# Kernel tuning notes

Measured on AMD Instinct MI355X. Metric: run time of the kernel, lower is better.

## Reference

```python
import jax, jax.numpy as jnp
import numpy as np

SINKHORN_ITERS = 5
EPS_CLAMP = 1e-8   # matches torch eps=1e-08 in unbalanced_optimal_transport
EPS_COS = 1e-6     # matches cosine_distance eps
EPS_DIV = 1e-6     # matches weighted_ref / rigid transform eps


def setup_inputs() -> dict:
    key = jax.random.key(0)
    k0, k1, k2, k3 = jax.random.split(key, 4)
    B, D, M, N = 32, 512, 1024, 1024
    return {
        "src_embedding": jax.random.normal(k0, (B, D, M), dtype=jnp.float32),
        "tgt_embedding": jax.random.normal(k1, (B, D, N), dtype=jnp.float32),
        "src": jax.random.normal(k2, (B, 3, M), dtype=jnp.float32),
        "tgt": jax.random.normal(k3, (B, 3, N), dtype=jnp.float32),
        "l": jnp.float32(1.0),    # learned scalar nn.Parameter
        "rho": jnp.float32(1.0),  # learned scalar nn.Parameter
    }


def reference(src_embedding, tgt_embedding, src, tgt, l, rho):
    # ---- batched cosine distance: C[b] = 1 - <x1, x2> / (|x1||x2|) ----
    x1 = jnp.swapaxes(src_embedding, 1, 2)  # (B, M, D)
    x2 = jnp.swapaxes(tgt_embedding, 1, 2)  # (B, N, D)
    w1 = jnp.linalg.norm(x1, axis=2, keepdims=True)  # (B, M, 1)
    w2 = jnp.linalg.norm(x2, axis=2, keepdims=True)  # (B, N, 1)
    denom = jnp.clip(w1 * jnp.swapaxes(w2, 1, 2), EPS_COS, None)
    C = 1.0 - jnp.einsum('bmd,bnd->bmn', x1, x2) / denom  # (B, M, N)

    # ---- batched unbalanced Sinkhorn (5 fixed iterations) ----
    B, M, N = C.shape
    a = jnp.float32(1.0 / M)
    b = jnp.float32(1.0 / N)
    K = jnp.exp(-C / jnp.clip(l, EPS_CLAMP, None))        # (B, M, N)
    fi = rho / jnp.clip(rho + l, EPS_CLAMP, None)
    v = jnp.full((B, N), b, dtype=C.dtype)
    u = jnp.full((B, M), a, dtype=C.dtype)
    for _ in range(SINKHORN_ITERS):
        u = (a / jnp.clip(jnp.einsum('bmn,bn->bm', K, v), EPS_CLAMP, None)) ** fi
        v = (b / jnp.clip(jnp.einsum('bmn,bm->bn', K, u), EPS_CLAMP, None)) ** fi
    P = u[:, :, None] * K * v[:, None, :]                  # transport plan (B, M, N)

    # ---- soft correspondences ----
    row = jnp.sum(P, axis=2)                               # (B, M)
    tgt_pts = jnp.swapaxes(tgt, 1, 2)                      # (B, N, 3)
    weighted_ref = jnp.einsum('bmn,bnd->bmd', P, tgt_pts) / (row[:, :, None] + EPS_DIV)

    # ---- weighted Kabsch rigid transform (batched 3x3 SVD) ----
    a_pts = jnp.swapaxes(src, 1, 2)                        # (B, M, 3)
    w = row[:, :, None] / (jnp.sum(row, axis=1)[:, None, None] + EPS_DIV)  # (B, M, 1)
    centroid_a = jnp.sum(a_pts * w, axis=1)                # (B, 3)
    centroid_b = jnp.sum(weighted_ref * w, axis=1)         # (B, 3)
    a_c = a_pts - centroid_a[:, None, :]
    b_c = weighted_ref - centroid_b[:, None, :]
    cov = jnp.einsum('bmi,bmj->bij', a_c, b_c * w)         # (B, 3, 3)

    U, S, Vh = jnp.linalg.svd(cov, full_matrices=True)
    V = jnp.swapaxes(Vh, 1, 2)                             # torch.svd returns V, not V^T
    Ut = jnp.swapaxes(U, 1, 2)
    rot_pos = V @ Ut
    rot_neg = V.at[:, :, 2].multiply(-1.0) @ Ut            # flip last column of V
    det = jnp.linalg.det(rot_pos)[:, None, None]
    R = jnp.where(det > 0, rot_pos, rot_neg)               # (B, 3, 3)
    t = -jnp.einsum('bij,bj->bi', R, centroid_a) + centroid_b  # (B, 3)
    return R, t, P
```

## Files before the change

kernel.cpp:

```cpp
#include <hip/hip_runtime.h>
#include <math.h>

#define BB 32
#define DD 512
#define MM 1024
#define NN 1024

typedef float f32x4 __attribute__((ext_vector_type(4)));
typedef _Float16 f16x8 __attribute__((ext_vector_type(8)));

__global__ __launch_bounds__(256)
void norms_init_kernel(const float* __restrict__ srcE, const float* __restrict__ tgtE,
                       float* __restrict__ w1, float* __restrict__ w2,
                       float* __restrict__ v, float* __restrict__ colsum)
{
    const int idx = blockIdx.x * 256 + threadIdx.x;
    const float* e; float* w; int r;
    if (idx < 32768) {
        e = srcE; w = w1; r = idx;
        v[idx] = 1.0f / 1024.0f;
        colsum[idx] = 0.0f;
    } else {
        e = tgtE; w = w2; r = idx - 32768;
    }
    const int b = r >> 10;
    const int m = r & 1023;
    const float* p = e + (size_t)b * (DD * MM) + m;
    float acc = 0.f;
    #pragma unroll 8
    for (int d = 0; d < DD; ++d) {
        const float x = p[(size_t)d * MM];
        acc = fmaf(x, x, acc);
    }
    w[r] = sqrtf(acc);
}

__global__ __launch_bounds__(256)
void gemm_kexp_kernel(const float* __restrict__ Ae, const float* __restrict__ Be,
                      const float* __restrict__ w1, const float* __restrict__ w2,
                      const float* __restrict__ lp, float* __restrict__ Kout)
{
    __shared__ _Float16 As[128 * 64];
    __shared__ _Float16 Bs[128 * 64];

    const int tid  = threadIdx.x;
    const int lane = tid & 63;
    const int wave = tid >> 6;
    const int m0 = blockIdx.x * 128;
    const int n0 = blockIdx.y * 128;
    const int b  = blockIdx.z;
    const int wm = (wave & 1) * 64;
    const int wn = (wave >> 1) * 64;
    const int m16  = lane & 15;
    const int quad = lane >> 4;

    const float* Ab = Ae + (size_t)b * DD * MM;
    const float* Bb = Be + (size_t)b * DD * NN;

    f32x4 acc[4][4];
    #pragma unroll
    for (int i = 0; i < 4; ++i)
        #pragma unroll
        for (int j = 0; j < 4; ++j)
            acc[i][j] = (f32x4){0.f, 0.f, 0.f, 0.f};

    const int sm = tid & 127;
    const int kh = tid >> 7;
    const int sw = sm & 7;
    const float* apBase = Ab + m0 + sm;
    const float* bpBase = Bb + n0 + sm;

    float av[4][8], bv[4][8];
    #pragma unroll
    for (int t = 0; t < 4; ++t) {
        const int kg = kh + 2 * t;
        const float* ap = apBase + (size_t)(kg * 8) * MM;
        const float* bp = bpBase + (size_t)(kg * 8) * NN;
        #pragma unroll
        for (int j = 0; j < 8; ++j) { av[t][j] = ap[(size_t)j * MM]; bv[t][j] = bp[(size_t)j * NN]; }
    }

    for (int kt = 0; kt < 8; ++kt) {
        f16x8 pa[4], pb[4];
        #pragma unroll
        for (int t = 0; t < 4; ++t)
            #pragma unroll
            for (int j = 0; j < 8; ++j) { pa[t][j] = (_Float16)av[t][j]; pb[t][j] = (_Float16)bv[t][j]; }
        if (kt) __syncthreads();
        #pragma unroll
        for (int t = 0; t < 4; ++t) {
            const int kg = kh + 2 * t;
            const int off = sm * 64 + ((kg ^ sw) << 3);
            *reinterpret_cast<f16x8*>(&As[off]) = pa[t];
            *reinterpret_cast<f16x8*>(&Bs[off]) = pb[t];
        }
        __syncthreads();
        if (kt < 7) {
            const size_t kbase = (size_t)(kt + 1) * 64;
            #pragma unroll
            for (int t = 0; t < 4; ++t) {
                const int kg = kh + 2 * t;
                const float* ap = apBase + (kbase + kg * 8) * MM;
                const float* bp = bpBase + (kbase + kg * 8) * NN;
                #pragma unroll
                for (int j = 0; j < 8; ++j) { av[t][j] = ap[(size_t)j * MM]; bv[t][j] = bp[(size_t)j * NN]; }
            }
        }
        #pragma unroll
        for (int ks = 0; ks < 2; ++ks) {
            const int kg = ks * 4 + quad;
            f16x8 af[4], bfr[4];
            #pragma unroll
            for (int i = 0; i < 4; ++i) {
                const int rm = wm + i * 16 + m16;
                af[i]  = *reinterpret_cast<const f16x8*>(&As[rm * 64 + ((kg ^ (rm & 7)) << 3)]);
                const int rn = wn + i * 16 + m16;
                bfr[i] = *reinterpret_cast<const f16x8*>(&Bs[rn * 64 + ((kg ^ (rn & 7)) << 3)]);
            }
            #pragma unroll
            for (int i = 0; i < 4; ++i)
                #pragma unroll
                for (int j = 0; j < 4; ++j)
                    acc[i][j] = __builtin_amdgcn_mfma_f32_16x16x32_f16(af[i], bfr[j], acc[i][j], 0, 0, 0);
        }
    }

    const float inv_l = 1.0f / fmaxf(lp[0], 1e-8f);
    float w2v[4];
    #pragma unroll
    for (int j = 0; j < 4; ++j) w2v[j] = w2[b * NN + n0 + wn + j * 16 + m16];
    float* Kb = Kout + ((size_t)b << 20);
    #pragma unroll
    for (int i = 0; i < 4; ++i) {
        #pragma unroll
        for (int r = 0; r < 4; ++r) {
            const int m = m0 + wm + i * 16 + quad * 4 + r;
            const float w1v = w1[b * MM + m];
            #pragma unroll
            for (int j = 0; j < 4; ++j) {
                const float dot = acc[i][j][r];
                const float den = fmaxf(w1v * w2v[j], 1e-6f);
                const float kv  = __expf((dot / den - 1.0f) * inv_l);
                Kb[(size_t)m * NN + (n0 + wn + j * 16 + m16)] = kv;
            }
        }
    }
}

__global__ __launch_bounds__(256)
void uv_fused_kernel(const float* __restrict__ Kmat, const float* __restrict__ v,
                     float* __restrict__ u, float* __restrict__ colsum,
                     const float* __restrict__ lp, const float* __restrict__ rp)
{
    const int ms = blockIdx.x;
    const int b  = blockIdx.y;
    const int wv = threadIdx.x >> 6, lane = threadIdx.x & 63;
    const float l = lp[0], rho = rp[0];
    const float fi = rho / fmaxf(rho + l, 1e-8f);

    const float4* vb = reinterpret_cast<const float4*>(v + (b << 10));
    float4 vreg[4];
    #pragma unroll
    for (int c = 0; c < 4; ++c) vreg[c] = vb[c * 64 + lane];

    float4 cacc[4];
    #pragma unroll
    for (int c = 0; c < 4; ++c) cacc[c] = (float4){0.f, 0.f, 0.f, 0.f};

    const int m0 = ms * 32 + wv * 8;
    const float4* Kb = reinterpret_cast<const float4*>(Kmat + ((size_t)b << 20));
    float* ub = u + (b << 10);

    #pragma unroll
    for (int g = 0; g < 2; ++g) {
        float4 k4[4][4];
        #pragma unroll
        for (int r = 0; r < 4; ++r) {
            const int m = m0 + g * 4 + r;
            const float4* row = Kb + (size_t)m * 256;
            #pragma unroll
            for (int c = 0; c < 4; ++c) k4[r][c] = row[c * 64 + lane];
        }
        float s[4];
        #pragma unroll
        for (int r = 0; r < 4; ++r) {
            float t = 0.f;
            #pragma unroll
            for (int c = 0; c < 4; ++c) {
                t = fmaf(k4[r][c].x, vreg[c].x, t);
                t = fmaf(k4[r][c].y, vreg[c].y, t);
                t = fmaf(k4[r][c].z, vreg[c].z, t);
                t = fmaf(k4[r][c].w, vreg[c].w, t);
            }
            s[r] = t;
        }
        #pragma unroll
        for (int off = 32; off > 0; off >>= 1)
            #pragma unroll
            for (int r = 0; r < 4; ++r) s[r] += __shfl_down(s[r], off);
        float um[4];
        #pragma unroll
        for (int r = 0; r < 4; ++r) {
            const float sv = __builtin_amdgcn_readfirstlane(s[r]);
            um[r] = __powf((1.0f / 1024.0f) / fmaxf(sv, 1e-8f), fi);
        }
        if (lane == 0) {
            #pragma unroll
            for (int r = 0; r < 4; ++r) ub[m0 + g * 4 + r] = um[r];
        }
        #pragma unroll
        for (int r = 0; r < 4; ++r)
            #pragma unroll
            for (int c = 0; c < 4; ++c) {
                cacc[c].x = fmaf(k4[r][c].x, um[r], cacc[c].x);
                cacc[c].y = fmaf(k4[r][c].y, um[r], cacc[c].y);
                cacc[c].z = fmaf(k4[r][c].z, um[r], cacc[c].z);
                cacc[c].w = fmaf(k4[r][c].w, um[r], cacc[c].w);
            }
    }

    __shared__ float4 red[4][256];
    #pragma unroll
    for (int c = 0; c < 4; ++c) red[wv][c * 64 + lane] = cacc[c];
    __syncthreads();
    const int t = threadIdx.x;
    float4 s4 = red[0][t];
    #pragma unroll
    for (int w = 1; w < 4; ++w) {
        s4.x += red[w][t].x; s4.y += red[w][t].y;
        s4.z += red[w][t].z; s4.w += red[w][t].w;
    }
    float* cs = colsum + (b << 10) + t * 4;
    atomicAdd(cs + 0, s4.x);
    atomicAdd(cs + 1, s4.y);
    atomicAdd(cs + 2, s4.z);
    atomicAdd(cs + 3, s4.w);
}

__global__ __launch_bounds__(256)
void v_finalize_kernel(float* __restrict__ colsum, float* __restrict__ v,
                       const float* __restrict__ lp, const float* __restrict__ rp)
{
    const int idx = blockIdx.x * 256 + threadIdx.x;
    const float s = colsum[idx];
    colsum[idx] = 0.0f;
    const float l = lp[0], rho = rp[0];
    const float fi = rho / fmaxf(rho + l, 1e-8f);
    v[idx] = __powf((1.0f / 1024.0f) / fmaxf(s, 1e-8f), fi);
}

__global__ __launch_bounds__(256)
void p_pass_kernel(float* __restrict__ Kmat, const float* __restrict__ u,
                   const float* __restrict__ v, const float* __restrict__ tgt,
                   float* __restrict__ rowb, float* __restrict__ wref)
{
    const int gid  = (blockIdx.x * 256 + threadIdx.x) >> 6;
    const int lane = threadIdx.x & 63;
    const int b = gid >> 10;
    float4* row = reinterpret_cast<float4*>(Kmat + ((size_t)gid << 10));
    const float4* vb = reinterpret_cast<const float4*>(v + (b << 10));
    const float4* tb = reinterpret_cast<const float4*>(tgt + (size_t)b * 3072);
    const float um = u[gid];
    float4 s4 = {0,0,0,0}, x4 = {0,0,0,0}, y4 = {0,0,0,0}, z4 = {0,0,0,0};
    #pragma unroll
    for (int it = 0; it < 4; ++it) {
        const int i = it * 64 + lane;
        const float4 k4 = row[i];
        const float4 v4 = vb[i];
        float4 p;
        p.x = um * k4.x * v4.x;
        p.y = um * k4.y * v4.y;
        p.z = um * k4.z * v4.z;
        p.w = um * k4.w * v4.w;
        row[i] = p;
        const float4 tx = tb[i], ty = tb[256 + i], tz = tb[512 + i];
        s4.x += p.x; s4.y += p.y; s4.z += p.z; s4.w += p.w;
        x4.x = fmaf(p.x, tx.x, x4.x); x4.y = fmaf(p.y, tx.y, x4.y);
        x4.z = fmaf(p.z, tx.z, x4.z); x4.w = fmaf(p.w, tx.w, x4.w);
        y4.x = fmaf(p.x, ty.x, y4.x); y4.y = fmaf(p.y, ty.y, y4.y);
        y4.z = fmaf(p.z, ty.z, y4.z); y4.w = fmaf(p.w, ty.w, y4.w);
        z4.x = fmaf(p.x, tz.x, z4.x); z4.y = fmaf(p.y, tz.y, z4.y);
        z4.z = fmaf(p.z, tz.z, z4.z); z4.w = fmaf(p.w, tz.w, z4.w);
    }
    float s = (s4.x + s4.y) + (s4.z + s4.w);
    float x = (x4.x + x4.y) + (x4.z + x4.w);
    float y = (y4.x + y4.y) + (y4.z + y4.w);
    float z = (z4.x + z4.y) + (z4.z + z4.w);
    #pragma unroll
    for (int off = 32; off > 0; off >>= 1) {
        s += __shfl_down(s, off);
        x += __shfl_down(x, off);
        y += __shfl_down(y, off);
        z += __shfl_down(z, off);
    }
    if (lane == 0) {
        rowb[gid] = s;
        const float inv = 1.0f / (s + 1e-6f);
        wref[gid * 3 + 0] = x * inv;
        wref[gid * 3 + 1] = y * inv;
        wref[gid * 3 + 2] = z * inv;
    }
}

__device__ __forceinline__ float block_reduce_sum(float x, float* lds4, int wv, int lane)
{
    #pragma unroll
    for (int off = 32; off > 0; off >>= 1) x += __shfl_down(x, off);
    __syncthreads();
    if (lane == 0) lds4[wv] = x;
    __syncthreads();
    return (lds4[0] + lds4[1]) + (lds4[2] + lds4[3]);
}

__global__ __launch_bounds__(256)
void kabsch_stats_kernel(const float* __restrict__ rowb, const float* __restrict__ wref,
                         const float* __restrict__ src, float* __restrict__ cov,
                         float* __restrict__ ca, float* __restrict__ cb)
{
    __shared__ float lds4[4];
    const int b = blockIdx.x, tid = threadIdx.x;
    const int wv = tid >> 6, lane = tid & 63;
    float r[4], w[4], ax[4], ay[4], az[4], bx[4], by[4], bz[4];
    float rsum = 0.f;
    #pragma unroll
    for (int i = 0; i < 4; ++i) {
        const int m = tid + 256 * i;
        r[i] = rowb[(b << 10) + m];
        rsum += r[i];
    }
    const float total = block_reduce_sum(rsum, lds4, wv, lane);
    const float inv = 1.0f / (total + 1e-6f);
    #pragma unroll
    for (int i = 0; i < 4; ++i) {
        const int m = tid + 256 * i;
        w[i]  = r[i] * inv;
        ax[i] = src[b * 3072 + m];
        ay[i] = src[b * 3072 + 1024 + m];
        az[i] = src[b * 3072 + 2048 + m];
        bx[i] = wref[((b << 10) + m) * 3 + 0];
        by[i] = wref[((b << 10) + m) * 3 + 1];
        bz[i] = wref[((b << 10) + m) * 3 + 2];
    }
    float cax = 0, cay = 0, caz = 0, cbx = 0, cby = 0, cbz = 0;
    #pragma unroll
    for (int i = 0; i < 4; ++i) {
        cax = fmaf(ax[i], w[i], cax); cay = fmaf(ay[i], w[i], cay); caz = fmaf(az[i], w[i], caz);
        cbx = fmaf(bx[i], w[i], cbx); cby = fmaf(by[i], w[i], cby); cbz = fmaf(bz[i], w[i], cbz);
    }
    cax = block_reduce_sum(cax, lds4, wv, lane);
    cay = block_reduce_sum(cay, lds4, wv, lane);
    caz = block_reduce_sum(caz, lds4, wv, lane);
    cbx = block_reduce_sum(cbx, lds4, wv, lane);
    cby = block_reduce_sum(cby, lds4, wv, lane);
    cbz = block_reduce_sum(cbz, lds4, wv, lane);
    float c[9] = {0,0,0,0,0,0,0,0,0};
    #pragma unroll
    for (int i = 0; i < 4; ++i) {
        const float dax = ax[i] - cax, day = ay[i] - cay, daz = az[i] - caz;
        const float dbx = (bx[i] - cbx) * w[i];
        const float dby = (by[i] - cby) * w[i];
        const float dbz = (bz[i] - cbz) * w[i];
        c[0] = fmaf(dax, dbx, c[0]); c[1] = fmaf(dax, dby, c[1]); c[2] = fmaf(dax, dbz, c[2]);
        c[3] = fmaf(day, dbx, c[3]); c[4] = fmaf(day, dby, c[4]); c[5] = fmaf(day, dbz, c[5]);
        c[6] = fmaf(daz, dbx, c[6]); c[7] = fmaf(daz, dby, c[7]); c[8] = fmaf(daz, dbz, c[8]);
    }
    #pragma unroll
    for (int k = 0; k < 9; ++k) c[k] = block_reduce_sum(c[k], lds4, wv, lane);
    if (tid == 0) {
        #pragma unroll
        for (int k = 0; k < 9; ++k) cov[b * 9 + k] = c[k];
        ca[b * 3 + 0] = cax; ca[b * 3 + 1] = cay; ca[b * 3 + 2] = caz;
        cb[b * 3 + 0] = cbx; cb[b * 3 + 1] = cby; cb[b * 3 + 2] = cbz;
    }
}

__device__ __forceinline__ void jrot_d(double S[3][3], double V[3][3], int p, int q)
{
    const double apq = S[p][q];
    if (fabs(apq) < 1e-300) return;
    const double theta = (S[q][q] - S[p][p]) / (2.0 * apq);
    const double tt = copysign(1.0, theta) / (fabs(theta) + sqrt(1.0 + theta * theta));
    const double c = 1.0 / sqrt(1.0 + tt * tt);
    const double s = tt * c;
    #pragma unroll
    for (int k = 0; k < 3; ++k) {
        const double skp = S[k][p], skq = S[k][q];
        S[k][p] = c * skp - s * skq;
        S[k][q] = s * skp + c * skq;
    }
    #pragma unroll
    for (int k = 0; k < 3; ++k) {
        const double spk = S[p][k], sqk = S[q][k];
        S[p][k] = c * spk - s * sqk;
        S[q][k] = s * spk + c * sqk;
    }
    #pragma unroll
    for (int k = 0; k < 3; ++k) {
        const double vkp = V[k][p], vkq = V[k][q];
        V[k][p] = c * vkp - s * vkq;
        V[k][q] = s * vkp + c * vkq;
    }
}

__global__ __launch_bounds__(64)
void svd_kernel(const float* __restrict__ cov, const float* __restrict__ ca,
                const float* __restrict__ cb, float* __restrict__ out)
{
    const int b = threadIdx.x;
    if (b >= 32) return;
    double A[3][3];
    #pragma unroll
    for (int i = 0; i < 3; ++i)
        #pragma unroll
        for (int j = 0; j < 3; ++j)
            A[i][j] = (double)cov[b * 9 + i * 3 + j];
    double S[3][3];
    #pragma unroll
    for (int i = 0; i < 3; ++i)
        #pragma unroll
        for (int j = 0; j < 3; ++j)
            S[i][j] = A[0][i] * A[0][j] + A[1][i] * A[1][j] + A[2][i] * A[2][j];
    double V[3][3] = {{1,0,0},{0,1,0},{0,0,1}};
    for (int sweep = 0; sweep < 8; ++sweep) {
        jrot_d(S, V, 0, 1);
        jrot_d(S, V, 0, 2);
        jrot_d(S, V, 1, 2);
    }
    int o0 = 0, o1 = 1, o2 = 2;
    double e0 = S[0][0], e1 = S[1][1], e2 = S[2][2];
    double tf; int ti;
    if (e0 < e1) { tf = e0; e0 = e1; e1 = tf; ti = o0; o0 = o1; o1 = ti; }
    if (e0 < e2) { tf = e0; e0 = e2; e2 = tf; ti = o0; o0 = o2; o2 = ti; }
    if (e1 < e2) { tf = e1; e1 = e2; e2 = tf; ti = o1; o1 = o2; o2 = ti; }
    double v1[3] = {V[0][o0], V[1][o0], V[2][o0]};
    double v2[3] = {V[0][o1], V[1][o1], V[2][o1]};
    double v3[3] = {V[0][o2], V[1][o2], V[2][o2]};
    double Av1[3], Av2[3];
    #pragma unroll
    for (int i = 0; i < 3; ++i) {
        Av1[i] = A[i][0] * v1[0] + A[i][1] * v1[1] + A[i][2] * v1[2];
        Av2[i] = A[i][0] * v2[0] + A[i][1] * v2[1] + A[i][2] * v2[2];
    }
    const double n1 = sqrt(Av1[0]*Av1[0] + Av1[1]*Av1[1] + Av1[2]*Av1[2]);
    const double in1 = 1.0 / fmax(n1, 1e-300);
    double u1[3] = {Av1[0]*in1, Av1[1]*in1, Av1[2]*in1};
    const double d12 = Av2[0]*u1[0] + Av2[1]*u1[1] + Av2[2]*u1[2];
    double u2[3] = {Av2[0] - d12*u1[0], Av2[1] - d12*u1[1], Av2[2] - d12*u1[2]};
    const double n2 = sqrt(u2[0]*u2[0] + u2[1]*u2[1] + u2[2]*u2[2]);
    const double in2 = 1.0 / fmax(n2, 1e-300);
    u2[0] *= in2; u2[1] *= in2; u2[2] *= in2;
    double u3[3] = {u1[1]*u2[2] - u1[2]*u2[1],
                    u1[2]*u2[0] - u1[0]*u2[2],
                    u1[0]*u2[1] - u1[1]*u2[0]};
    double R0[3][3];
    #pragma unroll
    for (int i = 0; i < 3; ++i)
        #pragma unroll
        for (int j = 0; j < 3; ++j)
            R0[i][j] = v1[i]*u1[j] + v2[i]*u2[j] + v3[i]*u3[j];
    const double det =
        R0[0][0]*(R0[1][1]*R0[2][2] - R0[1][2]*R0[2][1])
      - R0[0][1]*(R0[1][0]*R0[2][2] - R0[1][2]*R0[2][0])
      + R0[0][2]*(R0[1][0]*R0[2][1] - R0[1][1]*R0[2][0]);
    double Rm[3][3];
    if (det > 0.0) {
        #pragma unroll
        for (int i = 0; i < 3; ++i)
            #pragma unroll
            for (int j = 0; j < 3; ++j)
                Rm[i][j] = R0[i][j];
    } else {
        #pragma unroll
        for (int i = 0; i < 3; ++i)
            #pragma unroll
            for (int j = 0; j < 3; ++j)
                Rm[i][j] = R0[i][j] - 2.0 * v3[i] * u3[j];
    }
    const double cax = (double)ca[b*3+0], cay = (double)ca[b*3+1], caz = (double)ca[b*3+2];
    #pragma unroll
    for (int i = 0; i < 3; ++i)
        #pragma unroll
        for (int j = 0; j < 3; ++j)
            out[b * 9 + i * 3 + j] = (float)Rm[i][j];
    #pragma unroll
    for (int i = 0; i < 3; ++i)
        out[288 + b * 3 + i] = (float)((double)cb[b*3+i] - (Rm[i][0]*cax + Rm[i][1]*cay + Rm[i][2]*caz));
}

extern "C" void kernel_launch(void* const* d_in, const int* in_sizes, int n_in,
                              void* d_out, int out_size, void* d_ws, size_t ws_size,
                              hipStream_t stream)
{
    const float* srcE = (const float*)d_in[0];
    const float* tgtE = (const float*)d_in[1];
    const float* src  = (const float*)d_in[2];
    const float* tgt  = (const float*)d_in[3];
    const float* lp   = (const float*)d_in[4];
    const float* rp   = (const float*)d_in[5];
    float* out  = (float*)d_out;
    float* Pout = out + 384;

    float* ws     = (float*)d_ws;
    float* w1     = ws;
    float* w2     = ws + 32768;
    float* u      = ws + 65536;
    float* v      = ws + 98304;
    float* rowb   = ws + 131072;
    float* wref   = ws + 163840;
    float* colsum = ws + 262144;
    float* cov    = ws + 294912;
    float* ca     = ws + 295200;
    float* cb     = ws + 295296;

    norms_init_kernel<<<256, 256, 0, stream>>>(srcE, tgtE, w1, w2, v, colsum);
    gemm_kexp_kernel<<<dim3(8, 8, 32), 256, 0, stream>>>(srcE, tgtE, w1, w2, lp, Pout);
    for (int it = 0; it < 5; ++it) {
        uv_fused_kernel<<<dim3(32, 32), 256, 0, stream>>>(Pout, v, u, colsum, lp, rp);
        v_finalize_kernel<<<128, 256, 0, stream>>>(colsum, v, lp, rp);
    }
    p_pass_kernel<<<8192, 256, 0, stream>>>(Pout, u, v, tgt, rowb, wref);
    kabsch_stats_kernel<<<32, 256, 0, stream>>>(rowb, wref, src, cov, ca, cb);
    svd_kernel<<<1, 64, 0, stream>>>(cov, ca, cb, out);
}
```

Before: 574.6 us.

## Store Sinkhorn kernel matrix K as 16-bit fixed point inside the P buffer

The GEMM epilogue now quantizes K = exp(...) to unsigned 16-bit fixed point (scale 65535) and packs each row into the first half of the corresponding fp32 P row. The fused u/v Sinkhorn kernel and the P pass read these packed values, dequantize them with per-row and per-column scaling, and the P pass overwrites the row in place with fp32 P after a full wait on loads. This halves the bytes read from HBM in every Sinkhorn iteration and in the K write. The cost is quantization error in K, which loses relative precision for small K values, plus a more delicate in-place aliasing scheme.

```diff
diff --git a/kernel.cpp b/kernel.cpp
--- a/kernel.cpp
+++ b/kernel.cpp
@@ -8,6 +8,7 @@
 
 typedef float f32x4 __attribute__((ext_vector_type(4)));
 typedef _Float16 f16x8 __attribute__((ext_vector_type(8)));
+
 
 __global__ __launch_bounds__(256)
 void norms_init_kernel(const float* __restrict__ srcE, const float* __restrict__ tgtE,
@@ -129,19 +130,21 @@
     float w2v[4];
     #pragma unroll
     for (int j = 0; j < 4; ++j) w2v[j] = w2[b * NN + n0 + wn + j * 16 + m16];
-    float* Kb = Kout + ((size_t)b << 20);
     #pragma unroll
     for (int i = 0; i < 4; ++i) {
         #pragma unroll
         for (int r = 0; r < 4; ++r) {
             const int m = m0 + wm + i * 16 + quad * 4 + r;
             const float w1v = w1[b * MM + m];
+            unsigned short* rowp =
+                (unsigned short*)((char*)Kout + ((size_t)((b << 10) + m) << 12));
             #pragma unroll
             for (int j = 0; j < 4; ++j) {
                 const float dot = acc[i][j][r];
                 const float den = fmaxf(w1v * w2v[j], 1e-6f);
                 const float kv  = __expf((dot / den - 1.0f) * inv_l);
-                Kb[(size_t)m * NN + (n0 + wn + j * 16 + m16)] = kv;
+                rowp[n0 + wn + j * 16 + m16] =
+                    (unsigned short)fminf(fmaf(kv, 65535.0f, 0.5f), 65535.0f);
             }
         }
     }
@@ -157,80 +160,90 @@
     const int wv = threadIdx.x >> 6, lane = threadIdx.x & 63;
     const float l = lp[0], rho = rp[0];
     const float fi = rho / fmaxf(rho + l, 1e-8f);
-
-    const float4* vb = reinterpret_cast<const float4*>(v + (b << 10));
-    float4 vreg[4];
-    #pragma unroll
-    for (int c = 0; c < 4; ++c) vreg[c] = vb[c * 64 + lane];
-
-    float4 cacc[4];
-    #pragma unroll
-    for (int c = 0; c < 4; ++c) cacc[c] = (float4){0.f, 0.f, 0.f, 0.f};
-
     const int m0 = ms * 32 + wv * 8;
-    const float4* Kb = reinterpret_cast<const float4*>(Kmat + ((size_t)b << 20));
-    float* ub = u + (b << 10);
-
-    #pragma unroll
-    for (int g = 0; g < 2; ++g) {
-        float4 k4[4][4];
-        #pragma unroll
-        for (int r = 0; r < 4; ++r) {
-            const int m = m0 + g * 4 + r;
-            const float4* row = Kb + (size_t)m * 256;
-            #pragma unroll
-            for (int c = 0; c < 4; ++c) k4[r][c] = row[c * 64 + lane];
+    const int gid0 = (b << 10) + m0;
+
+    uint4 ku[8][2];
+    #pragma unroll
+    for (int r = 0; r < 8; ++r) {
+        const uint4* kr = (const uint4*)((const char*)Kmat + ((size_t)(gid0 + r) << 12));
+        ku[r][0] = kr[lane];
+        ku[r][1] = kr[64 + lane];
+    }
+    const float4* vb4 = (const float4*)(v + (b << 10));
+    float4 vv[4];
+    vv[0] = vb4[2 * lane];       vv[1] = vb4[2 * lane + 1];
+    vv[2] = vb4[128 + 2 * lane]; vv[3] = vb4[129 + 2 * lane];
+
+    float s[8];
+    #pragma unroll
+    for (int r = 0; r < 8; ++r) {
+        float t = 0.f;
+        #pragma unroll
+        for (int c = 0; c < 2; ++c) {
+            const uint4 q = ku[r][c];
+            const float4 va = vv[2 * c], vb2 = vv[2 * c + 1];
+            t = fmaf((float)(q.x & 0xffffu), va.x, t);
+            t = fmaf((float)(q.x >> 16),     va.y, t);
+            t = fmaf((float)(q.y & 0xffffu), va.z, t);
+            t = fmaf((float)(q.y >> 16),     va.w, t);
+            t = fmaf((float)(q.z & 0xffffu), vb2.x, t);
+            t = fmaf((float)(q.z >> 16),     vb2.y, t);
+            t = fmaf((float)(q.w & 0xffffu), vb2.z, t);
+            t = fmaf((float)(q.w >> 16),     vb2.w, t);
         }
-        float s[4];
-        #pragma unroll
-        for (int r = 0; r < 4; ++r) {
-            float t = 0.f;
-            #pragma unroll
-            for (int c = 0; c < 4; ++c) {
-                t = fmaf(k4[r][c].x, vreg[c].x, t);
-                t = fmaf(k4[r][c].y, vreg[c].y, t);
-                t = fmaf(k4[r][c].z, vreg[c].z, t);
-                t = fmaf(k4[r][c].w, vreg[c].w, t);
-            }
-            s[r] = t;
+        s[r] = t;
+    }
+    #pragma unroll
+    for (int off = 32; off > 0; off >>= 1)
+        #pragma unroll
+        for (int r = 0; r < 8; ++r) s[r] += __shfl_down(s[r], off);
+    float um[8];
+    #pragma unroll
+    for (int r = 0; r < 8; ++r) {
+        const float sv = __builtin_amdgcn_readfirstlane(s[r]) * (1.0f / 65535.0f);
+        um[r] = __powf((1.0f / 1024.0f) / fmaxf(sv, 1e-8f), fi);
+    }
+    if (lane == 0) {
+        float* ub = u + (b << 10);
+        #pragma unroll
+        for (int r = 0; r < 8; ++r) ub[m0 + r] = um[r];
+    }
+
+    float cacc[16];
+    #pragma unroll
+    for (int j = 0; j < 16; ++j) cacc[j] = 0.f;
+    #pragma unroll
+    for (int r = 0; r < 8; ++r) {
+        const float umr = um[r];
+        #pragma unroll
+        for (int c = 0; c < 2; ++c) {
+            const uint4 q = ku[r][c];
+            float* cc = &cacc[8 * c];
+            cc[0] = fmaf((float)(q.x & 0xffffu), umr, cc[0]);
+            cc[1] = fmaf((float)(q.x >> 16),     umr, cc[1]);
+            cc[2] = fmaf((float)(q.y & 0xffffu), umr, cc[2]);
+            cc[3] = fmaf((float)(q.y >> 16),     umr, cc[3]);
+            cc[4] = fmaf((float)(q.z & 0xffffu), umr, cc[4]);
+            cc[5] = fmaf((float)(q.z >> 16),     umr, cc[5]);
+            cc[6] = fmaf((float)(q.w & 0xffffu), umr, cc[6]);
+            cc[7] = fmaf((float)(q.w >> 16),     umr, cc[7]);
         }
-        #pragma unroll
-        for (int off = 32; off > 0; off >>= 1)
-            #pragma unroll
-            for (int r = 0; r < 4; ++r) s[r] += __shfl_down(s[r], off);
-        float um[4];
-        #pragma unroll
-        for (int r = 0; r < 4; ++r) {
-            const float sv = __builtin_amdgcn_readfirstlane(s[r]);
-            um[r] = __powf((1.0f / 1024.0f) / fmaxf(sv, 1e-8f), fi);
-        }
-        if (lane == 0) {
-            #pragma unroll
-            for (int r = 0; r < 4; ++r) ub[m0 + g * 4 + r] = um[r];
-        }
-        #pragma unroll
-        for (int r = 0; r < 4; ++r)
-            #pragma unroll
-            for (int c = 0; c < 4; ++c) {
-                cacc[c].x = fmaf(k4[r][c].x, um[r], cacc[c].x);
-                cacc[c].y = fmaf(k4[r][c].y, um[r], cacc[c].y);
-                cacc[c].z = fmaf(k4[r][c].z, um[r], cacc[c].z);
-                cacc[c].w = fmaf(k4[r][c].w, um[r], cacc[c].w);
-            }
-    }
-
-    __shared__ float4 red[4][256];
-    #pragma unroll
-    for (int c = 0; c < 4; ++c) red[wv][c * 64 + lane] = cacc[c];
+    }
+    __shared__ float red[4][1024];
+    *reinterpret_cast<float4*>(&red[wv][8 * lane])           = make_float4(cacc[0],  cacc[1],  cacc[2],  cacc[3]);
+    *reinterpret_cast<float4*>(&red[wv][8 * lane + 4])       = make_float4(cacc[4],  cacc[5],  cacc[6],  cacc[7]);
+    *reinterpret_cast<float4*>(&red[wv][512 + 8 * lane])     = make_float4(cacc[8],  cacc[9],  cacc[10], cacc[11]);
+    *reinterpret_cast<float4*>(&red[wv][512 + 8 * lane + 4]) = make_float4(cacc[12], cacc[13], cacc[14], cacc[15]);
     __syncthreads();
     const int t = threadIdx.x;
-    float4 s4 = red[0][t];
+    float4 s4 = *reinterpret_cast<const float4*>(&red[0][4 * t]);
     #pragma unroll
     for (int w = 1; w < 4; ++w) {
-        s4.x += red[w][t].x; s4.y += red[w][t].y;
-        s4.z += red[w][t].z; s4.w += red[w][t].w;
-    }
-    float* cs = colsum + (b << 10) + t * 4;
+        const float4 rw = *reinterpret_cast<const float4*>(&red[w][4 * t]);
+        s4.x += rw.x; s4.y += rw.y; s4.z += rw.z; s4.w += rw.w;
+    }
+    float* cs = colsum + (b << 10) + 4 * t;
     atomicAdd(cs + 0, s4.x);
     atomicAdd(cs + 1, s4.y);
     atomicAdd(cs + 2, s4.z);
@@ -242,7 +255,7 @@
                        const float* __restrict__ lp, const float* __restrict__ rp)
 {
     const int idx = blockIdx.x * 256 + threadIdx.x;
-    const float s = colsum[idx];
+    const float s = colsum[idx] * (1.0f / 65535.0f);
     colsum[idx] = 0.0f;
     const float l = lp[0], rho = rp[0];
     const float fi = rho / fmaxf(rho + l, 1e-8f);
@@ -257,35 +270,58 @@
     const int gid  = (blockIdx.x * 256 + threadIdx.x) >> 6;
     const int lane = threadIdx.x & 63;
     const int b = gid >> 10;
-    float4* row = reinterpret_cast<float4*>(Kmat + ((size_t)gid << 10));
-    const float4* vb = reinterpret_cast<const float4*>(v + (b << 10));
-    const float4* tb = reinterpret_cast<const float4*>(tgt + (size_t)b * 3072);
-    const float um = u[gid];
-    float4 s4 = {0,0,0,0}, x4 = {0,0,0,0}, y4 = {0,0,0,0}, z4 = {0,0,0,0};
-    #pragma unroll
-    for (int it = 0; it < 4; ++it) {
-        const int i = it * 64 + lane;
-        const float4 k4 = row[i];
-        const float4 v4 = vb[i];
-        float4 p;
-        p.x = um * k4.x * v4.x;
-        p.y = um * k4.y * v4.y;
-        p.z = um * k4.z * v4.z;
-        p.w = um * k4.w * v4.w;
-        row[i] = p;
-        const float4 tx = tb[i], ty = tb[256 + i], tz = tb[512 + i];
-        s4.x += p.x; s4.y += p.y; s4.z += p.z; s4.w += p.w;
-        x4.x = fmaf(p.x, tx.x, x4.x); x4.y = fmaf(p.y, tx.y, x4.y);
-        x4.z = fmaf(p.z, tx.z, x4.z); x4.w = fmaf(p.w, tx.w, x4.w);
-        y4.x = fmaf(p.x, ty.x, y4.x); y4.y = fmaf(p.y, ty.y, y4.y);
-        y4.z = fmaf(p.z, ty.z, y4.z); y4.w = fmaf(p.w, ty.w, y4.w);
-        z4.x = fmaf(p.x, tz.x, z4.x); z4.y = fmaf(p.y, tz.y, z4.y);
-        z4.z = fmaf(p.z, tz.z, z4.z); z4.w = fmaf(p.w, tz.w, z4.w);
-    }
-    float s = (s4.x + s4.y) + (s4.z + s4.w);
-    float x = (x4.x + x4.y) + (x4.z + x4.w);
-    float y = (y4.x + y4.y) + (y4.z + y4.w);
-    float z = (z4.x + z4.y) + (z4.z + z4.w);
+    char* rowbase = (char*)Kmat + ((size_t)gid << 12);
+    const uint4* kr = (const uint4*)rowbase;
+    uint4 ku[2];
+    ku[0] = kr[lane];
+    ku[1] = kr[64 + lane];
+    const float4* vb = (const float4*)(v + (b << 10));
+    const float4* tb = (const float4*)(tgt + (size_t)b * 3072);
+    const float um_s = u[gid] * (1.0f / 65535.0f);
+    float4 vv[4], txa[4], tya[4], tza[4];
+    vv[0]  = vb[2 * lane];        vv[1]  = vb[2 * lane + 1];
+    vv[2]  = vb[128 + 2 * lane];  vv[3]  = vb[129 + 2 * lane];
+    txa[0] = tb[2 * lane];        txa[1] = tb[2 * lane + 1];
+    txa[2] = tb[128 + 2 * lane];  txa[3] = tb[129 + 2 * lane];
+    tya[0] = tb[256 + 2 * lane];  tya[1] = tb[257 + 2 * lane];
+    tya[2] = tb[384 + 2 * lane];  tya[3] = tb[385 + 2 * lane];
+    tza[0] = tb[512 + 2 * lane];  tza[1] = tb[513 + 2 * lane];
+    tza[2] = tb[640 + 2 * lane];  tza[3] = tb[641 + 2 * lane];
+    asm volatile("s_waitcnt vmcnt(0)" ::: "memory");
+    float4* prow = (float4*)rowbase;
+    float s = 0.f, x = 0.f, y = 0.f, z = 0.f;
+    #pragma unroll
+    for (int c = 0; c < 2; ++c) {
+        const uint4 q = ku[c];
+        const float k0 = (float)(q.x & 0xffffu), k1 = (float)(q.x >> 16);
+        const float k2 = (float)(q.y & 0xffffu), k3 = (float)(q.y >> 16);
+        const float k4 = (float)(q.z & 0xffffu), k5 = (float)(q.z >> 16);
+        const float k6 = (float)(q.w & 0xffffu), k7 = (float)(q.w >> 16);
+        const float4 va = vv[2 * c], vb2 = vv[2 * c + 1];
+        float4 pa, pb;
+        pa.x = um_s * k0 * va.x;  pa.y = um_s * k1 * va.y;
+        pa.z = um_s * k2 * va.z;  pa.w = um_s * k3 * va.w;
+        pb.x = um_s * k4 * vb2.x; pb.y = um_s * k5 * vb2.y;
+        pb.z = um_s * k6 * vb2.z; pb.w = um_s * k7 * vb2.w;
+        prow[c * 128 + 2 * lane]     = pa;
+        prow[c * 128 + 2 * lane + 1] = pb;
+        s += (pa.x + pa.y) + (pa.z + pa.w) + (pb.x + pb.y) + (pb.z + pb.w);
+        const float4 x0 = txa[2 * c], x1 = txa[2 * c + 1];
+        const float4 y0 = tya[2 * c], y1 = tya[2 * c + 1];
+        const float4 z0 = tza[2 * c], z1 = tza[2 * c + 1];
+        x = fmaf(pa.x, x0.x, x); x = fmaf(pa.y, x0.y, x);
+        x = fmaf(pa.z, x0.z, x); x = fmaf(pa.w, x0.w, x);
+        x = fmaf(pb.x, x1.x, x); x = fmaf(pb.y, x1.y, x);
+        x = fmaf(pb.z, x1.z, x); x = fmaf(pb.w, x1.w, x);
+        y = fmaf(pa.x, y0.x, y); y = fmaf(pa.y, y0.y, y);
+        y = fmaf(pa.z, y0.z, y); y = fmaf(pa.w, y0.w, y);
+        y = fmaf(pb.x, y1.x, y); y = fmaf(pb.y, y1.y, y);
+        y = fmaf(pb.z, y1.z, y); y = fmaf(pb.w, y1.w, y);
+        z = fmaf(pa.x, z0.x, z); z = fmaf(pa.y, z0.y, z);
+        z = fmaf(pa.z, z0.z, z); z = fmaf(pa.w, z0.w, z);
+        z = fmaf(pb.x, z1.x, z); z = fmaf(pb.y, z1.y, z);
+        z = fmaf(pb.z, z1.z, z); z = fmaf(pb.w, z1.w, z);
+    }
     #pragma unroll
     for (int off = 32; off > 0; off >>= 1) {
         s += __shfl_down(s, off);
```

After: 553.2 us. 3.7% less time.
